# Kernel optimization log

Measured on AMD Instinct MI355X. Metric: run time of the kernel, lower is better.

The kernel has to match this reference:

```python
import jax, jax.numpy as jnp
import numpy as np

N_BOXES = 512
NUM_CLASSES = 151
IN_DIM = 4096
NMS_THRESH = 0.3


def setup_inputs() -> dict:
    key = jax.random.key(0)
    k1, k2, k3, k4 = jax.random.split(key, 4)
    obj_fmap = jax.random.normal(k1, (N_BOXES, IN_DIM), dtype=jnp.float32)
    W = jax.random.normal(k2, (IN_DIM, NUM_CLASSES), dtype=jnp.float32) * 0.02
    b = jnp.zeros((NUM_CLASSES,), dtype=jnp.float32)
    xy = jax.random.uniform(k3, (N_BOXES, NUM_CLASSES, 2), minval=0.0, maxval=800.0)
    wh = jax.random.uniform(k4, (N_BOXES, NUM_CLASSES, 2), minval=20.0, maxval=220.0)
    boxes_per_cls = jnp.concatenate([xy, xy + wh], axis=-1).astype(jnp.float32)
    return {"obj_fmap": obj_fmap, "boxes_per_cls": boxes_per_cls, "W": W, "b": b}


def nms_overlaps(boxes):
    # boxes: [N, C, 4] xyxy -> per-class pairwise IoU [N, N, C]
    x1, y1, x2, y2 = boxes[..., 0], boxes[..., 1], boxes[..., 2], boxes[..., 3]
    areas = (x2 - x1 + 1.0) * (y2 - y1 + 1.0)  # [N, C]
    ix1 = jnp.maximum(x1[:, None, :], x1[None, :, :])  # [N, N, C]
    iy1 = jnp.maximum(y1[:, None, :], y1[None, :, :])
    ix2 = jnp.minimum(x2[:, None, :], x2[None, :, :])
    iy2 = jnp.minimum(y2[:, None, :], y2[None, :, :])
    iw = jnp.clip(ix2 - ix1 + 1.0, 0.0)
    ih = jnp.clip(iy2 - iy1 + 1.0, 0.0)
    inter = iw * ih
    union = areas[:, None, :] + areas[None, :, :] - inter
    return inter / union


def greedy_nms_decode(obj_dists, boxes_per_cls, thresh):
    # Sequential greedy commitment: repeatedly take global argmax over the
    # [N, C] score matrix, commit that class to that box, zero out the same
    # class for overlapping boxes, and retire the committed box.
    N, C = obj_dists.shape
    is_overlap = nms_overlaps(boxes_per_cls) >= thresh  # [N, N, C] bool
    scores = jax.nn.softmax(obj_dists, axis=1)
    scores = scores.at[:, 0].set(0.0)  # never pick background

    def step(carry, _):
        scores, commits = carry
        flat = jnp.argmax(scores)
        box = flat // C
        cls = flat % C
        commits = commits.at[box].set(cls)
        col = jnp.where(is_overlap[box, :, cls], 0.0, scores[:, cls])
        scores = scores.at[:, cls].set(col)
        scores = scores.at[box].set(-1.0)
        return (scores, commits), None

    init = (scores, jnp.zeros((N,), dtype=jnp.int32))
    (_, commits), _ = jax.lax.scan(step, init, None, length=N)
    return commits


def reference(obj_fmap, boxes_per_cls, W, b):
    # out_obj linear head
    obj_dists = obj_fmap @ W + b  # [N, C]
    # sgdet eval path: greedy NMS-style class commitment
    obj_preds = greedy_nms_decode(obj_dists, boxes_per_cls, NMS_THRESH)
    return (obj_dists, obj_preds)
```

## Files before the change

### kernel.cpp

```cpp
#include <hip/hip_runtime.h>
#include <limits.h>

#pragma clang fp contract(off)

#define NB 512
#define NC 151
#define KDIM 4096
#define KS 8
#define KCH (KDIM/KS)
#define GRB 4
#define PST 152
#define NK 64
#define NL 16
#define CMX 16
#define RMX 64
#define NMS_TH 0.3f

typedef unsigned long long ull;

__device__ __forceinline__ bool overlap_ge(const float4& c, const float4& o) {
  float areaC = (c.z - c.x + 1.0f) * (c.w - c.y + 1.0f);
  float areaJ = (o.z - o.x + 1.0f) * (o.w - o.y + 1.0f);
  float iw = fminf(c.z, o.z) - fmaxf(c.x, o.x) + 1.0f;
  float ih = fminf(c.w, o.w) - fmaxf(c.y, o.y) + 1.0f;
  iw = fmaxf(iw, 0.0f); ih = fmaxf(ih, 0.0f);
  float inter = iw * ih;
  float uni = areaC + areaJ - inter;
  return inter / uni >= NMS_TH;
}

__device__ __forceinline__ bool mbit(const unsigned m[5], int c) {
  bool r = false;
#pragma unroll
  for (int k = 0; k < 5; ++k) r = (k == (c >> 5)) ? (((m[k] >> (c & 31)) & 1u) != 0) : r;
  return r;
}

__device__ __forceinline__ ull shflx_u64(ull v, int m) {
  int lo = (int)(unsigned)(v & 0xFFFFFFFFull);
  int hi = (int)(unsigned)(v >> 32);
  lo = __shfl_xor(lo, m, 64);
  hi = __shfl_xor(hi, m, 64);
  return ((ull)(unsigned)hi << 32) | (unsigned)lo;
}

__device__ __forceinline__ ull readlane_u64(ull v, int t) {
  int lo = __builtin_amdgcn_readlane((int)(unsigned)(v & 0xFFFFFFFFull), t);
  int hi = __builtin_amdgcn_readlane((int)(unsigned)(v >> 32), t);
  return ((ull)(unsigned)hi << 32) | (unsigned)lo;
}

#define TPB_GEMM ((NB / GRB) * KS)
#define NTR ((NB * NC + 191) / 192)
__global__ __launch_bounds__(192) void gemm_fused(
    const float* __restrict__ A, const float* __restrict__ W,
    const float* __restrict__ boxes, float* __restrict__ part, float* __restrict__ bt)
{
  if (blockIdx.x >= TPB_GEMM) {
    int i = (blockIdx.x - TPB_GEMM) * 192 + threadIdx.x;
    if (i < NB * NC) {
      int r = i / NC, c = i - r * NC;
      float4 v = *(const float4*)(boxes + (size_t)i * 4);
      *(float4*)(bt + ((size_t)c * NB + r) * 4) = v;
    }
    return;
  }
  __shared__ float sA[GRB * KCH];
  int rb = blockIdx.x >> 3, ks = blockIdx.x & 7;
  const float* Ab = A + (size_t)rb * GRB * KDIM + (size_t)ks * KCH;
  for (int i = threadIdx.x; i < GRB * (KCH / 4); i += 192) {
    int r = i >> 7;
    int k4 = i & 127;
    *(float4*)(sA + r * KCH + k4 * 4) = *(const float4*)(Ab + (size_t)r * KDIM + k4 * 4);
  }
  __syncthreads();
  int c = threadIdx.x;
  if (c < NC) {
    const float* wp = W + (size_t)ks * KCH * NC + c;
    float acc[GRB];
#pragma unroll
    for (int r = 0; r < GRB; ++r) acc[r] = 0.f;
    float w0 = wp[0], w1 = wp[NC], w2 = wp[2 * NC], w3 = wp[3 * NC];
    for (int k4 = 0; k4 < KCH / 4; ++k4) {
      int kn = (k4 + 1 < KCH / 4) ? (k4 + 1) : k4;
      const float* q = wp + (size_t)(4 * kn) * NC;
      float n0 = q[0], n1 = q[NC], n2 = q[2 * NC], n3 = q[3 * NC];
#pragma unroll
      for (int r = 0; r < GRB; ++r) {
        float4 a = *(const float4*)(sA + r * KCH + k4 * 4);
        acc[r] = fmaf(a.x, w0, acc[r]);
        acc[r] = fmaf(a.y, w1, acc[r]);
        acc[r] = fmaf(a.z, w2, acc[r]);
        acc[r] = fmaf(a.w, w3, acc[r]);
      }
      w0 = n0; w1 = n1; w2 = n2; w3 = n3;
    }
    float* o = part + ((size_t)ks * NB + (size_t)rb * GRB) * PST + c;
#pragma unroll
    for (int r = 0; r < GRB; ++r) o[(size_t)r * PST] = acc[r];
  }
}

__global__ __launch_bounds__(64) void prep_kernel(
    const float* __restrict__ part, const float* __restrict__ bias,
    float* __restrict__ out, float* __restrict__ lp, float* __restrict__ tl)
{
  const int j = blockIdx.x;
  const int l = threadIdx.x;
  const int c0 = l, c1 = l + 64, c2 = l + 128;
  const bool v2 = (c2 < NC);

  float x0 = 0.f, x1 = 0.f, x2 = 0.f;
#pragma unroll
  for (int ks = 0; ks < KS; ++ks) {
    const float* pb = part + ((size_t)ks * NB + j) * PST;
    x0 += pb[c0];
    x1 += pb[c1];
    if (v2) x2 += pb[c2];
  }
  x0 += bias[c0];
  x1 += bias[c1];
  if (v2) x2 += bias[c2]; else x2 = -3.4e38f;

  float* orow = out + (size_t)j * NC;
  orow[c0] = x0;
  orow[c1] = x1;
  if (v2) orow[c2] = x2;

  float m_ = fmaxf(x0, fmaxf(x1, x2));
#pragma unroll
  for (int d = 1; d < 64; d <<= 1) m_ = fmaxf(m_, __shfl_xor(m_, d, 64));

  float e0 = expf(x0 - m_), e1 = expf(x1 - m_), e2 = expf(x2 - m_);
  float s_ = e0 + e1 + e2;
#pragma unroll
  for (int d = 1; d < 64; d <<= 1) s_ += __shfl_xor(s_, d, 64);

  float p0 = (c0 == 0) ? 0.f : e0 / s_;
  float p1 = e1 / s_;
  float p2 = e2 / s_;

  float* pr = lp + (size_t)j * PST;
  pr[c0] = p0;
  pr[c1] = p1;
  if (c2 < PST) pr[c2] = v2 ? p2 : 0.f;

  auto mk = [&](float p, int c) -> ull {
    if (!(p > 0.f)) return 0ull;
    unsigned u = __float_as_uint(p) ^ 0x80000000u;
    return ((ull)u << 32) | (unsigned)(255 - c);
  };
  ull k0 = mk(p0, c0), k1 = mk(p1, c1), k2 = v2 ? mk(p2, c2) : 0ull;
  { ull a = k0 > k1 ? k0 : k1, b = k0 > k1 ? k1 : k0; k0 = a; k1 = b; }
  { ull a = k1 > k2 ? k1 : k2, b = k1 > k2 ? k2 : k1; k1 = a; k2 = b; }
  { ull a = k0 > k1 ? k0 : k1, b = k0 > k1 ? k1 : k0; k0 = a; k1 = b; }

  ull mykey = 0ull;
#pragma unroll
  for (int t = 0; t < NL; ++t) {
    ull g = k0;
#pragma unroll
    for (int d = 1; d < 64; d <<= 1) {
      ull o = shflx_u64(g, d);
      g = g > o ? g : o;
    }
    if (g != 0ull && k0 == g) { k0 = k1; k1 = k2; k2 = 0ull; }
    if (l == t) mykey = g;
  }

  if (l < NL) {
    float lv; int lc;
    if (mykey == 0ull) { lv = -3.4e38f; lc = 0; }
    else {
      lv = __uint_as_float((unsigned)(mykey >> 32) ^ 0x80000000u);
      lc = 255 - (int)(mykey & 0xFFu);
    }
    float* tr = tl + (size_t)j * (2 * NL);
    tr[l] = lv;
    tr[NL + l] = __int_as_float(lc);
  }
}

__global__ __launch_bounds__(192) void gemm_full(
    const float* __restrict__ A, const float* __restrict__ W,
    const float* __restrict__ bias, float* __restrict__ out)
{
  int c = threadIdx.x;
  int r0 = blockIdx.x * 4;
  if (c >= NC) return;
  const float* a = A + (size_t)r0 * KDIM;
  const float* wp = W + c;
  float a0 = 0.f, a1 = 0.f, a2 = 0.f, a3 = 0.f;
#pragma unroll 8
  for (int k = 0; k < KDIM; ++k) {
    float w = wp[(size_t)k * NC];
    a0 = fmaf(a[k],            w, a0);
    a1 = fmaf(a[k + KDIM],     w, a1);
    a2 = fmaf(a[k + 2 * KDIM], w, a2);
    a3 = fmaf(a[k + 3 * KDIM], w, a3);
  }
  float bb = bias[c];
  out[(size_t)(r0 + 0) * NC + c] = a0 + bb;
  out[(size_t)(r0 + 1) * NC + c] = a1 + bb;
  out[(size_t)(r0 + 2) * NC + c] = a2 + bb;
  out[(size_t)(r0 + 3) * NC + c] = a3 + bb;
}

template <bool FAST>
__global__ __launch_bounds__(512) void decode_kernel(
    const float* __restrict__ lp, const float* __restrict__ tl,
    const float* __restrict__ boxes ,
    float* __restrict__ commits)
{
  __shared__ __align__(16) ull bufA[NB];
  __shared__ __align__(16) ull bufB[NB];
  __shared__ __align__(16) int swin[NK];
  __shared__ ull smask[NK];
  __shared__ unsigned slog[NB];
  __shared__ int cls_cnt[NC];
  __shared__ unsigned short cls_ref[NC][CMX];
  __shared__ unsigned short P[NB];
  __shared__ ull nkk[RMX];
  __shared__ int nkr[RMX], nko[RMX], nkc[RMX];
  __shared__ int m_cnt;
  __shared__ ull sred[8];
  const int j = threadIdx.x;
  const int lane = j & 63;
  const int w = j >> 6;

  auto bload = [&](int cls, int row) -> float4 {
    return FAST ? *(const float4*)(boxes + ((size_t)cls * NB + row) * 4)
                : *(const float4*)(boxes + ((size_t)row * NC + cls) * 4);
  };
  auto enc = [&](float v, int cls) -> ull {
    unsigned u = __float_as_uint(v);
    u ^= (u & 0x80000000u) ? 0xFFFFFFFFu : 0x80000000u;
    return ((ull)u << 32) | (unsigned)(0xFFFFFFFFu - (unsigned)(j * NC + cls));
  };

  if (j < NC) cls_cnt[j] = 0;

  float lv[NL]; int lc[NL];
  float m_ = 0.f, s_ = 1.f;
  const float* xr = FAST ? (lp + (size_t)j * PST) : (lp + (size_t)j * NC);

  if (FAST) {
    const float4* tl4 = (const float4*)(tl + (size_t)j * (2 * NL));
#pragma unroll
    for (int q = 0; q < NL / 4; ++q) {
      float4 v = tl4[q];
      lv[4 * q] = v.x; lv[4 * q + 1] = v.y; lv[4 * q + 2] = v.z; lv[4 * q + 3] = v.w;
    }
#pragma unroll
    for (int q = 0; q < NL / 4; ++q) {
      float4 v = tl4[NL / 4 + q];
      lc[4 * q] = __float_as_int(v.x); lc[4 * q + 1] = __float_as_int(v.y);
      lc[4 * q + 2] = __float_as_int(v.z); lc[4 * q + 3] = __float_as_int(v.w);
    }
  } else {
#pragma unroll
    for (int t = 0; t < NL; ++t) { lv[t] = -3.4e38f; lc[t] = 0; }
    m_ = xr[0];
    for (int c = 1; c < NC; ++c) m_ = fmaxf(m_, xr[c]);
    s_ = 0.f;
    for (int c = 0; c < NC; ++c) s_ += expf(xr[c] - m_);
    for (int c = 1; c < NC; ++c) {
      float v = expf(xr[c] - m_) / s_;
      if (v > lv[NL - 1]) {
        lv[NL - 1] = v; lc[NL - 1] = c;
#pragma unroll
        for (int q = NL - 1; q > 0; --q) {
          if (lv[q] > lv[q - 1]) {
            float tv = lv[q]; lv[q] = lv[q - 1]; lv[q - 1] = tv;
            int tc = lc[q]; lc[q] = lc[q - 1]; lc[q - 1] = tc;
          }
        }
      }
    }
  }

  float rowmax; int argcls; bool zstuck = false;
  if (lv[0] > 0.f) { rowmax = lv[0]; argcls = lc[0]; }
  else { rowmax = 0.f; argcls = 0; zstuck = true; }

  bool retired = false;
  int commitcls = 0;
  int ncom = 0;
  int base = 0;
  int logcnt = 0;
  int flip = 0;
  bool eg = false;

  auto fullsort = [&](ull key) {
    __syncthreads();
    bufB[j] = key;
    __syncthreads();
    int rank = 0;
#pragma unroll 8
    for (int q = 0; q < NB; ++q) rank += (bufB[q] > key) ? 1 : 0;
    bufA[rank] = key;
    P[j] = (unsigned short)rank;
    __syncthreads();
  };

  fullsort(enc(rowmax, argcls));

  while (ncom < NB) {
    ull* Lc = flip ? bufB : bufA;
    ull* Ln = flip ? bufA : bufB;
    int bsz = NB - base; if (bsz > NK) bsz = NK;
    int myprev = (!retired && !zstuck) ? cls_cnt[argcls] : 0;

    if (j < bsz) {
      ull k = Lc[base + j];
      unsigned f = 0xFFFFFFFFu - (unsigned)k;
      int row = (int)(f / (unsigned)NC);
      swin[j] = (row << 8) | (int)(f - (unsigned)row * (unsigned)NC);
      smask[j] = 0ull;
    }
    if (j == 0) m_cnt = 0;
    if (w == 7) {
      volatile int* pb = (volatile int*)slog;
      int t0 = pb[(lane & 31) * 16];
      int t1 = pb[(lane & 31) * 16 + 1];
      asm volatile("" :: "v"(t0), "v"(t1));
    }
    __syncthreads();

    {
      int t = j >> 3, sb = (j & 7) * 8;
      if (t < bsz) {
        int pT = swin[t];
        int cT = pT & 255, rT = pT >> 8;
        int4 sA4 = *(const int4*)&swin[sb];
        int4 sB4 = *(const int4*)&swin[sb + 4];
        int ss[8] = {sA4.x, sA4.y, sA4.z, sA4.w, sB4.x, sB4.y, sB4.z, sB4.w};
        ull myc = 0ull;
#pragma unroll
        for (int u = 0; u < 8; ++u) {
          int s = sb + u;
          if (s < t && (ss[u] & 255) == cT) {
            float4 bs = bload(cT, ss[u] >> 8);
            float4 btx = bload(cT, rT);
            if (overlap_ge(bs, btx)) myc |= (1ull << s);
          }
        }
        if (myc) atomicOr(&smask[t], myc);
      }
    }
    __syncthreads();

    int p;
    {
      ull kv = (lane < bsz) ? Lc[base + lane] : 0ull;
      ull sm = (lane < bsz) ? smask[lane] : 0ull;
      ull okm = __ballot((lane < bsz) && ((unsigned)(kv >> 32) > 0x80000000u));
      ull anyc = __ballot(sm != 0ull);
      if (!(okm & 1ull)) {
        p = 0; eg = true;
      } else if (anyc == 0ull) {
        ull inv = ~okm;
        if (inv == 0ull) p = 64;
        else p = (int)__ffsll((long long)inv) - 1;
        eg = (p < bsz);
      } else {
        ull valid = 1ull; p = 1;
#pragma unroll
        for (int t = 1; t < NK; ++t) {
          ull cm = readlane_u64(sm, t);
          bool ok = (p == t) && ((okm >> t) & 1ull) && ((cm & valid) == 0ull);
          if (ok) { valid |= (1ull << t); p = t + 1; }
        }
        eg = (p < bsz) && !((okm >> p) & 1ull);
      }
    }

    if (j < p) {
      unsigned e = (unsigned)swin[j];
      slog[logcnt + j] = e;
      int c = (int)(e & 255u);
      int old = atomicAdd(&cls_cnt[c], 1);
      if (old < CMX) cls_ref[c][old] = (unsigned short)(logcnt + j);
    }
    __syncthreads();
    logcnt += p;

    bool chg = false; ull nkey = 0ull;
    if (!retired) {
      int mypos = (int)P[j];
      if (mypos >= base && mypos < base + p) {
        retired = true; commitcls = argcls;
      } else if (!zstuck) {
        bool supp = false;
        int nowc = cls_cnt[argcls];
        if (nowc > myprev) {
          float4 ob = bload(argcls, j);
          if (nowc <= CMX) {
#pragma unroll 1
            for (int q = myprev; q < nowc && !supp; ++q) {
              unsigned e = slog[cls_ref[argcls][q]];
              if (overlap_ge(bload(argcls, (int)(e >> 8)), ob)) supp = true;
            }
          } else {
#pragma unroll 1
            for (int q = logcnt - p; q < logcnt && !supp; ++q) {
              unsigned e = slog[q];
              if ((int)(e & 255u) == argcls &&
                  overlap_ge(bload(argcls, (int)(e >> 8)), ob)) supp = true;
            }
          }
        }
        if (supp) {
          bool found = false;
#pragma unroll 1
          for (int t = 0; t < NL && !found; ++t) {
            if (!(lv[t] > 0.f)) break;
            int c = lc[t];
            int cnt = cls_cnt[c];
            bool bad = false;
            if (cnt > 0) {
              float4 ob2 = bload(c, j);
              if (cnt <= CMX) {
                for (int q = 0; q < cnt && !bad; ++q) {
                  unsigned e = slog[cls_ref[c][q]];
                  if (overlap_ge(bload(c, (int)(e >> 8)), ob2)) bad = true;
                }
              } else {
                for (int q = 0; q < logcnt && !bad; ++q) {
                  unsigned e = slog[q];
                  if ((int)(e & 255u) == c &&
                      overlap_ge(bload(c, (int)(e >> 8)), ob2)) bad = true;
                }
              }
            }
            if (!bad) { rowmax = lv[t]; argcls = c; found = true; }
          }
          if (!found) {
            unsigned msk[5] = {0, 0, 0, 0, 0};
            for (int q = 0; q < logcnt; ++q) {
              unsigned e = slog[q];
              int c = (int)(e & 255u), r = (int)(e >> 8);
              if (r != j && !mbit(msk, c)) {
                if (overlap_ge(bload(c, r), bload(c, j))) {
#pragma unroll
                  for (int k5b = 0; k5b < 5; ++k5b)
                    if (k5b == (c >> 5)) msk[k5b] |= (1u << (c & 31));
                }
              }
            }
            float bm = -3.4e38f; int ba = 0;
            if (FAST) {
              for (int c4 = 0; c4 < PST / 4; ++c4) {
                float4 v4 = *(const float4*)(xr + c4 * 4);
                int c = c4 * 4;
                float vals[4] = {v4.x, v4.y, v4.z, v4.w};
#pragma unroll
                for (int u = 0; u < 4; ++u) {
                  int cc = c + u;
                  float v = mbit(msk, cc) ? 0.f : vals[u];
                  if (v > bm) { bm = v; ba = cc; }
                }
              }
            } else {
              for (int c = 0; c < NC; ++c) {
                float v;
                if (c == 0) v = 0.f;
                else v = mbit(msk, c) ? 0.f : (expf(xr[c] - m_) / s_);
                if (v > bm) { bm = v; ba = c; }
              }
            }
            rowmax = bm; argcls = ba;
            if (!(bm > 0.f)) zstuck = true;
          }
          chg = true; nkey = enc(rowmax, argcls);
        }
      }
    }
    if (chg) {
      int i = atomicAdd(&m_cnt, 1);
      if (i < RMX) { nkk[i] = nkey; nkr[i] = j; nko[i] = (int)P[j]; nkc[i] = 0; }
    }
    __syncthreads();

    int m = m_cnt;
    base += p; ncom += p;
    if (eg) break;
    if (m == 0) continue;

    if (m <= RMX) {
      bool haveslot = (j >= base);
      ull myk = 0ull; bool isrem = false; int rb_ = 0;
      if (haveslot) {
        myk = Lc[j];
#pragma unroll 1
        for (int i = 0; i < m; ++i) { int op = nko[i]; isrem |= (op == j); rb_ += (op < j) ? 1 : 0; }
      }
#pragma unroll 1
      for (int i = 0; i < m; ++i) {
        ull b = __ballot(haveslot && !isrem && (myk > nkk[i]));
        if (lane == 0 && b) atomicAdd(&nkc[i], (int)__popcll(b));
      }
      if (haveslot && !isrem) {
        int nb_ = 0;
#pragma unroll 1
        for (int i = 0; i < m; ++i) nb_ += (nkk[i] > myk) ? 1 : 0;
        int np = j - rb_ + nb_;
        Ln[np] = myk;
        if (myk != 0ull) {
          unsigned f = 0xFFFFFFFFu - (unsigned)myk;
          int rr = (int)(f / (unsigned)NC);
          P[rr] = (unsigned short)np;
        }
      }
      __syncthreads();
      if (j < m) {
        ull ki = nkk[j]; int gt = 0;
#pragma unroll 1
        for (int i = 0; i < m; ++i) gt += (nkk[i] > ki) ? 1 : 0;
        int np = base + nkc[j] + gt;
        Ln[np] = ki;
        P[nkr[j]] = (unsigned short)np;
      }
      __syncthreads();
      flip ^= 1;
    } else {
      fullsort(enc(rowmax, argcls));
      flip = 0;
      base = 0;
    }
  }

  if (ncom < NB) {
    unsigned msk[5] = {0, 0, 0, 0, 0};
    int post_min = INT_MAX;
    bool ret = false; int ccls = commitcls;
    for (int q = 0; q < logcnt; ++q) {
      unsigned e = slog[q];
      int r = (int)(e >> 8), c = (int)(e & 255u);
      if (j == r) { ret = true; ccls = c; post_min = INT_MAX; }
      else {
        if (overlap_ge(bload(c, r), bload(c, j))) {
          if (ret) post_min = (c < post_min) ? c : post_min;
          else {
#pragma unroll
            for (int k5b = 0; k5b < 5; ++k5b) if (k5b == (c >> 5)) msk[k5b] |= (1u << (c & 31));
          }
        }
      }
    }
    retired = ret; if (ret) commitcls = ccls;
    if (retired) {
      rowmax = (post_min != INT_MAX) ? 0.0f : -1.0f;
      argcls = (post_min != INT_MAX) ? post_min : 0;
    } else {
      float bm = -3.4e38f; int ba = 0;
      if (FAST) {
        for (int c4 = 0; c4 < PST / 4; ++c4) {
          float4 v4 = *(const float4*)(xr + c4 * 4);
          int c = c4 * 4;
          float vals[4] = {v4.x, v4.y, v4.z, v4.w};
#pragma unroll
          for (int u = 0; u < 4; ++u) {
            int cc = c + u;
            float v = mbit(msk, cc) ? 0.f : vals[u];
            if (v > bm) { bm = v; ba = cc; }
          }
        }
      } else {
        for (int c = 0; c < NC; ++c) {
          float v;
          if (c == 0) v = 0.f;
          else v = mbit(msk, c) ? 0.f : (expf(xr[c] - m_) / s_);
          if (v > bm) { bm = v; ba = c; }
        }
      }
      rowmax = bm; argcls = ba;
    }

    while (ncom < NB) {
      ull k = enc(rowmax, argcls);
#pragma unroll
      for (int dd = 32; dd >= 1; dd >>= 1) {
        ull o = shflx_u64(k, dd);
        k = k > o ? k : o;
      }
      __syncthreads();
      if (lane == 0) sred[w] = k;
      if (w == 7) {
        volatile int* pb = (volatile int*)slog;
        int t0 = pb[(lane & 31) * 16];
        asm volatile("" :: "v"(t0));
      }
      __syncthreads();
      ull g = sred[0];
#pragma unroll
      for (int q = 1; q < 8; ++q) { ull t = sred[q]; g = g > t ? g : t; }
      unsigned f = 0xFFFFFFFFu - (unsigned)g;
      int row = (int)(f / (unsigned)NC);
      int cls = (int)(f - (unsigned)row * (unsigned)NC);
      float4 cb = bload(cls, row);
      float4 ob = bload(cls, j);
      if (j == row) {
        retired = true; commitcls = cls;
        rowmax = -1.0f; argcls = 0;
        post_min = INT_MAX;
      } else if (overlap_ge(cb, ob)) {
        if (retired) {
          post_min = (cls < post_min) ? cls : post_min;
          rowmax = 0.0f; argcls = post_min;
        }
      }
      ++ncom;
    }
  }

  commits[j] = (float)commitcls;
}

extern "C" void kernel_launch(void* const* d_in, const int* in_sizes, int n_in,
                              void* d_out, int out_size, void* d_ws, size_t ws_size,
                              hipStream_t stream) {
  const float* A     = (const float*)d_in[0];
  const float* boxes = (const float*)d_in[1];
  const float* W     = (const float*)d_in[2];
  const float* bias  = (const float*)d_in[3];
  float* out = (float*)d_out;

  const size_t np = (size_t)KS * NB * PST;
  const size_t nl = (size_t)NB * PST;
  const size_t nt = (size_t)NB * (2 * NL);
  const size_t nb = (size_t)NC * NB * 4;
  const size_t need = (np + nl + nt + nb) * 4;

  if (ws_size >= need) {
    float* part = (float*)d_ws;
    float* lp   = part + np;
    float* tl   = lp + nl;
    float* bt   = tl + nt;
    gemm_fused<<<TPB_GEMM + NTR, 192, 0, stream>>>(A, W, boxes, part, bt);
    prep_kernel<<<NB, 64, 0, stream>>>(part, bias, out, lp, tl);
    decode_kernel<true><<<1, NB, 0, stream>>>(lp, tl, bt, out + NB * NC);
  } else {
    gemm_full<<<NB / 4, 192, 0, stream>>>(A, W, bias, out);
    decode_kernel<false><<<1, NB, 0, stream>>>(out, nullptr, boxes, out + NB * NC);
  }
}
```

Before: 139.7 us.

## Fuse GEMM, softmax prep and greedy decode into one cooperative kernel

Replaces the three-kernel sequence (split-K GEMM plus box transpose, prep/softmax/top-16, single-block decode) with one cooperative launch of 512 blocks of 512 threads. Grid-wide syncs separate the phases. The GEMM phase is retiled to 8 rows per block with register prefetch of W. This removes two kernel-launch gaps, but it adds grid-sync cost and leaves 511 blocks idle during the serial decode. If the cooperative launch fails, the old three-kernel path runs instead.

```diff
diff --git a/kernel.cpp b/kernel.cpp
--- a/kernel.cpp
+++ b/kernel.cpp
@@ -1,7 +1,10 @@
 #include <hip/hip_runtime.h>
+#include <hip/hip_cooperative_groups.h>
 #include <limits.h>
 
 #pragma clang fp contract(off)
+
+namespace cg = cooperative_groups;
 
 #define NB 512
 #define NC 151
@@ -48,6 +51,509 @@
   int lo = __builtin_amdgcn_readlane((int)(unsigned)(v & 0xFFFFFFFFull), t);
   int hi = __builtin_amdgcn_readlane((int)(unsigned)(v >> 32), t);
   return ((ull)(unsigned)hi << 32) | (unsigned)lo;
+}
+
+__global__ __launch_bounds__(512) void fused_kernel(
+    const float* __restrict__ A, const float* __restrict__ W,
+    const float* __restrict__ boxes, const float* __restrict__ bias,
+    float* __restrict__ part, float* __restrict__ lp, float* __restrict__ tl,
+    float* __restrict__ bt, float* __restrict__ out)
+{
+  __shared__ float sA[8 * KCH];
+  __shared__ __align__(16) ull bufA[NB];
+  __shared__ __align__(16) ull bufB[NB];
+  __shared__ __align__(16) int swin[NK];
+  __shared__ ull smask[NK];
+  __shared__ unsigned slog[NB];
+  __shared__ int cls_cnt[NC];
+  __shared__ unsigned short cls_ref[NC][CMX];
+  __shared__ unsigned short P[NB];
+  __shared__ ull nkk[RMX];
+  __shared__ int nkr[RMX], nko[RMX], nkc[RMX];
+  __shared__ int m_cnt;
+  __shared__ ull sred[8];
+
+  const int bid = blockIdx.x;
+  const int t = threadIdx.x;
+
+  {
+    int rb = bid >> 3, ks = bid & 7;
+    const float* Ab = A + (size_t)rb * 8 * KDIM + (size_t)ks * KCH;
+    for (int i = t; i < 8 * (KCH / 4); i += 512) {
+      int r = i >> 7, k4 = i & 127;
+      *(float4*)(sA + r * KCH + k4 * 4) = *(const float4*)(Ab + (size_t)r * KDIM + k4 * 4);
+    }
+    int ti = bid * 512 + t;
+    if (ti < NB * NC) {
+      int r = ti / NC, c = ti - r * NC;
+      float4 v = *(const float4*)(boxes + (size_t)ti * 4);
+      *(float4*)(bt + ((size_t)c * NB + r) * 4) = v;
+    }
+    __syncthreads();
+    int c = t & 255, h = t >> 8;
+    if (c < NC) {
+      const float* wp = W + (size_t)ks * KCH * NC + c;
+      float acc[4];
+#pragma unroll
+      for (int r = 0; r < 4; ++r) acc[r] = 0.f;
+      const float* sb = sA + (size_t)(h * 4) * KCH;
+      float w0 = wp[0], w1 = wp[NC], w2 = wp[2 * NC], w3 = wp[3 * NC];
+      for (int k4 = 0; k4 < KCH / 4; ++k4) {
+        int kn = (k4 + 1 < KCH / 4) ? (k4 + 1) : k4;
+        const float* q = wp + (size_t)(4 * kn) * NC;
+        float n0 = q[0], n1 = q[NC], n2 = q[2 * NC], n3 = q[3 * NC];
+#pragma unroll
+        for (int r = 0; r < 4; ++r) {
+          float4 a = *(const float4*)(sb + r * KCH + k4 * 4);
+          acc[r] = fmaf(a.x, w0, acc[r]);
+          acc[r] = fmaf(a.y, w1, acc[r]);
+          acc[r] = fmaf(a.z, w2, acc[r]);
+          acc[r] = fmaf(a.w, w3, acc[r]);
+        }
+        w0 = n0; w1 = n1; w2 = n2; w3 = n3;
+      }
+      float* o = part + ((size_t)ks * NB + (size_t)rb * 8 + h * 4) * PST + c;
+#pragma unroll
+      for (int r = 0; r < 4; ++r) o[(size_t)r * PST] = acc[r];
+    }
+  }
+
+  cg::this_grid().sync();
+
+  if (bid < 64) {
+    const int wv = t >> 6, l = t & 63;
+    const int j = bid * 8 + wv;
+    const int c0 = l, c1 = l + 64, c2 = l + 128;
+    const bool v2 = (c2 < NC);
+
+    float x0 = 0.f, x1 = 0.f, x2 = 0.f;
+#pragma unroll
+    for (int ks = 0; ks < KS; ++ks) {
+      const float* pb = part + ((size_t)ks * NB + j) * PST;
+      x0 += pb[c0];
+      x1 += pb[c1];
+      if (v2) x2 += pb[c2];
+    }
+    x0 += bias[c0];
+    x1 += bias[c1];
+    if (v2) x2 += bias[c2]; else x2 = -3.4e38f;
+
+    float* orow = out + (size_t)j * NC;
+    orow[c0] = x0;
+    orow[c1] = x1;
+    if (v2) orow[c2] = x2;
+
+    float m_ = fmaxf(x0, fmaxf(x1, x2));
+#pragma unroll
+    for (int d = 1; d < 64; d <<= 1) m_ = fmaxf(m_, __shfl_xor(m_, d, 64));
+
+    float e0 = expf(x0 - m_), e1 = expf(x1 - m_), e2 = expf(x2 - m_);
+    float s_ = e0 + e1 + e2;
+#pragma unroll
+    for (int d = 1; d < 64; d <<= 1) s_ += __shfl_xor(s_, d, 64);
+
+    float p0 = (c0 == 0) ? 0.f : e0 / s_;
+    float p1 = e1 / s_;
+    float p2 = e2 / s_;
+
+    float* pr = lp + (size_t)j * PST;
+    pr[c0] = p0;
+    pr[c1] = p1;
+    if (c2 < PST) pr[c2] = v2 ? p2 : 0.f;
+
+    auto mk = [&](float p, int c) -> ull {
+      if (!(p > 0.f)) return 0ull;
+      unsigned u = __float_as_uint(p) ^ 0x80000000u;
+      return ((ull)u << 32) | (unsigned)(255 - c);
+    };
+    ull k0 = mk(p0, c0), k1 = mk(p1, c1), k2 = v2 ? mk(p2, c2) : 0ull;
+    { ull a = k0 > k1 ? k0 : k1, b = k0 > k1 ? k1 : k0; k0 = a; k1 = b; }
+    { ull a = k1 > k2 ? k1 : k2, b = k1 > k2 ? k2 : k1; k1 = a; k2 = b; }
+    { ull a = k0 > k1 ? k0 : k1, b = k0 > k1 ? k1 : k0; k0 = a; k1 = b; }
+
+    ull mykey = 0ull;
+#pragma unroll
+    for (int tt = 0; tt < NL; ++tt) {
+      ull g = k0;
+#pragma unroll
+      for (int d = 1; d < 64; d <<= 1) {
+        ull o = shflx_u64(g, d);
+        g = g > o ? g : o;
+      }
+      if (g != 0ull && k0 == g) { k0 = k1; k1 = k2; k2 = 0ull; }
+      if (l == tt) mykey = g;
+    }
+
+    if (l < NL) {
+      float lvv; int lcc;
+      if (mykey == 0ull) { lvv = -3.4e38f; lcc = 0; }
+      else {
+        lvv = __uint_as_float((unsigned)(mykey >> 32) ^ 0x80000000u);
+        lcc = 255 - (int)(mykey & 0xFFu);
+      }
+      float* tr = tl + (size_t)j * (2 * NL);
+      tr[l] = lvv;
+      tr[NL + l] = __int_as_float(lcc);
+    }
+  }
+
+  cg::this_grid().sync();
+
+  if (bid != 0) return;
+  {
+    const int j = t;
+    const int lane = j & 63;
+    const int w = j >> 6;
+    float* commits = out + NB * NC;
+
+    auto bload = [&](int cls, int row) -> float4 {
+      return *(const float4*)(bt + ((size_t)cls * NB + row) * 4);
+    };
+    auto enc = [&](float v, int cls) -> ull {
+      unsigned u = __float_as_uint(v);
+      u ^= (u & 0x80000000u) ? 0xFFFFFFFFu : 0x80000000u;
+      return ((ull)u << 32) | (unsigned)(0xFFFFFFFFu - (unsigned)(j * NC + cls));
+    };
+
+    if (j < NC) cls_cnt[j] = 0;
+
+    float lv[NL]; int lc[NL];
+    const float* xr = lp + (size_t)j * PST;
+
+    {
+      const float4* tl4 = (const float4*)(tl + (size_t)j * (2 * NL));
+#pragma unroll
+      for (int q = 0; q < NL / 4; ++q) {
+        float4 v = tl4[q];
+        lv[4 * q] = v.x; lv[4 * q + 1] = v.y; lv[4 * q + 2] = v.z; lv[4 * q + 3] = v.w;
+      }
+#pragma unroll
+      for (int q = 0; q < NL / 4; ++q) {
+        float4 v = tl4[NL / 4 + q];
+        lc[4 * q] = __float_as_int(v.x); lc[4 * q + 1] = __float_as_int(v.y);
+        lc[4 * q + 2] = __float_as_int(v.z); lc[4 * q + 3] = __float_as_int(v.w);
+      }
+    }
+
+    float rowmax; int argcls; bool zstuck = false;
+    if (lv[0] > 0.f) { rowmax = lv[0]; argcls = lc[0]; }
+    else { rowmax = 0.f; argcls = 0; zstuck = true; }
+
+    bool retired = false;
+    int commitcls = 0;
+    int ncom = 0;
+    int base = 0;
+    int logcnt = 0;
+    int flip = 0;
+    bool eg = false;
+
+    auto fullsort = [&](ull key) {
+      __syncthreads();
+      bufB[j] = key;
+      __syncthreads();
+      int rank = 0;
+#pragma unroll 8
+      for (int q = 0; q < NB; ++q) rank += (bufB[q] > key) ? 1 : 0;
+      bufA[rank] = key;
+      P[j] = (unsigned short)rank;
+      __syncthreads();
+    };
+
+    fullsort(enc(rowmax, argcls));
+
+    while (ncom < NB) {
+      ull* Lc = flip ? bufB : bufA;
+      ull* Ln = flip ? bufA : bufB;
+      int bsz = NB - base; if (bsz > NK) bsz = NK;
+      int myprev = (!retired && !zstuck) ? cls_cnt[argcls] : 0;
+
+      if (j < bsz) {
+        ull k = Lc[base + j];
+        unsigned f = 0xFFFFFFFFu - (unsigned)k;
+        int row = (int)(f / (unsigned)NC);
+        swin[j] = (row << 8) | (int)(f - (unsigned)row * (unsigned)NC);
+        smask[j] = 0ull;
+      }
+      if (j == 0) m_cnt = 0;
+      if (w == 7) {
+        volatile int* pb = (volatile int*)slog;
+        int t0 = pb[(lane & 31) * 16];
+        int t1 = pb[(lane & 31) * 16 + 1];
+        asm volatile("" :: "v"(t0), "v"(t1));
+      }
+      __syncthreads();
+
+      {
+        int tt = j >> 3, sb = (j & 7) * 8;
+        if (tt < bsz) {
+          int pT = swin[tt];
+          int cT = pT & 255, rT = pT >> 8;
+          int4 sA4 = *(const int4*)&swin[sb];
+          int4 sB4 = *(const int4*)&swin[sb + 4];
+          int ss[8] = {sA4.x, sA4.y, sA4.z, sA4.w, sB4.x, sB4.y, sB4.z, sB4.w};
+          ull myc = 0ull;
+#pragma unroll
+          for (int u = 0; u < 8; ++u) {
+            int s = sb + u;
+            if (s < tt && (ss[u] & 255) == cT) {
+              float4 bs = bload(cT, ss[u] >> 8);
+              float4 btx = bload(cT, rT);
+              if (overlap_ge(bs, btx)) myc |= (1ull << s);
+            }
+          }
+          if (myc) atomicOr(&smask[tt], myc);
+        }
+      }
+      __syncthreads();
+
+      int p;
+      {
+        ull kv = (lane < bsz) ? Lc[base + lane] : 0ull;
+        ull sm = (lane < bsz) ? smask[lane] : 0ull;
+        ull okm = __ballot((lane < bsz) && ((unsigned)(kv >> 32) > 0x80000000u));
+        ull anyc = __ballot(sm != 0ull);
+        if (!(okm & 1ull)) {
+          p = 0; eg = true;
+        } else if (anyc == 0ull) {
+          ull inv = ~okm;
+          if (inv == 0ull) p = 64;
+          else p = (int)__ffsll((long long)inv) - 1;
+          eg = (p < bsz);
+        } else {
+          ull valid = 1ull; p = 1;
+#pragma unroll
+          for (int tt = 1; tt < NK; ++tt) {
+            ull cm = readlane_u64(sm, tt);
+            bool ok = (p == tt) && ((okm >> tt) & 1ull) && ((cm & valid) == 0ull);
+            if (ok) { valid |= (1ull << tt); p = tt + 1; }
+          }
+          eg = (p < bsz) && !((okm >> p) & 1ull);
+        }
+      }
+
+      if (j < p) {
+        unsigned e = (unsigned)swin[j];
+        slog[logcnt + j] = e;
+        int c = (int)(e & 255u);
+        int old = atomicAdd(&cls_cnt[c], 1);
+        if (old < CMX) cls_ref[c][old] = (unsigned short)(logcnt + j);
+      }
+      __syncthreads();
+      logcnt += p;
+
+      bool chg = false; ull nkey = 0ull;
+      if (!retired) {
+        int mypos = (int)P[j];
+        if (mypos >= base && mypos < base + p) {
+          retired = true; commitcls = argcls;
+        } else if (!zstuck) {
+          bool supp = false;
+          int nowc = cls_cnt[argcls];
+          if (nowc > myprev) {
+            float4 ob = bload(argcls, j);
+            if (nowc <= CMX) {
+#pragma unroll 1
+              for (int q = myprev; q < nowc && !supp; ++q) {
+                unsigned e = slog[cls_ref[argcls][q]];
+                if (overlap_ge(bload(argcls, (int)(e >> 8)), ob)) supp = true;
+              }
+            } else {
+#pragma unroll 1
+              for (int q = logcnt - p; q < logcnt && !supp; ++q) {
+                unsigned e = slog[q];
+                if ((int)(e & 255u) == argcls &&
+                    overlap_ge(bload(argcls, (int)(e >> 8)), ob)) supp = true;
+              }
+            }
+          }
+          if (supp) {
+            bool found = false;
+#pragma unroll 1
+            for (int tt = 0; tt < NL && !found; ++tt) {
+              if (!(lv[tt] > 0.f)) break;
+              int c = lc[tt];
+              int cnt = cls_cnt[c];
+              bool bad = false;
+              if (cnt > 0) {
+                float4 ob2 = bload(c, j);
+                if (cnt <= CMX) {
+                  for (int q = 0; q < cnt && !bad; ++q) {
+                    unsigned e = slog[cls_ref[c][q]];
+                    if (overlap_ge(bload(c, (int)(e >> 8)), ob2)) bad = true;
+                  }
+                } else {
+                  for (int q = 0; q < logcnt && !bad; ++q) {
+                    unsigned e = slog[q];
+                    if ((int)(e & 255u) == c &&
+                        overlap_ge(bload(c, (int)(e >> 8)), ob2)) bad = true;
+                  }
+                }
+              }
+              if (!bad) { rowmax = lv[tt]; argcls = c; found = true; }
+            }
+            if (!found) {
+              unsigned msk[5] = {0, 0, 0, 0, 0};
+              for (int q = 0; q < logcnt; ++q) {
+                unsigned e = slog[q];
+                int c = (int)(e & 255u), r = (int)(e >> 8);
+                if (r != j && !mbit(msk, c)) {
+                  if (overlap_ge(bload(c, r), bload(c, j))) {
+#pragma unroll
+                    for (int k5b = 0; k5b < 5; ++k5b)
+                      if (k5b == (c >> 5)) msk[k5b] |= (1u << (c & 31));
+                  }
+                }
+              }
+              float bm = -3.4e38f; int ba = 0;
+              for (int c4 = 0; c4 < PST / 4; ++c4) {
+                float4 v4 = *(const float4*)(xr + c4 * 4);
+                int c = c4 * 4;
+                float vals[4] = {v4.x, v4.y, v4.z, v4.w};
+#pragma unroll
+                for (int u = 0; u < 4; ++u) {
+                  int cc = c + u;
+                  float v = mbit(msk, cc) ? 0.f : vals[u];
+                  if (v > bm) { bm = v; ba = cc; }
+                }
+              }
+              rowmax = bm; argcls = ba;
+              if (!(bm > 0.f)) zstuck = true;
+            }
+            chg = true; nkey = enc(rowmax, argcls);
+          }
+        }
+      }
+      if (chg) {
+        int i = atomicAdd(&m_cnt, 1);
+        if (i < RMX) { nkk[i] = nkey; nkr[i] = j; nko[i] = (int)P[j]; nkc[i] = 0; }
+      }
+      __syncthreads();
+
+      int m = m_cnt;
+      base += p; ncom += p;
+      if (eg) break;
+      if (m == 0) continue;
+
+      if (m <= RMX) {
+        bool haveslot = (j >= base);
+        ull myk = 0ull; bool isrem = false; int rb_ = 0;
+        if (haveslot) {
+          myk = Lc[j];
+#pragma unroll 1
+          for (int i = 0; i < m; ++i) { int op = nko[i]; isrem |= (op == j); rb_ += (op < j) ? 1 : 0; }
+        }
+#pragma unroll 1
+        for (int i = 0; i < m; ++i) {
+          ull b = __ballot(haveslot && !isrem && (myk > nkk[i]));
+          if (lane == 0 && b) atomicAdd(&nkc[i], (int)__popcll(b));
+        }
+        if (haveslot && !isrem) {
+          int nb_ = 0;
+#pragma unroll 1
+          for (int i = 0; i < m; ++i) nb_ += (nkk[i] > myk) ? 1 : 0;
+          int np = j - rb_ + nb_;
+          Ln[np] = myk;
+          if (myk != 0ull) {
+            unsigned f = 0xFFFFFFFFu - (unsigned)myk;
+            int rr = (int)(f / (unsigned)NC);
+            P[rr] = (unsigned short)np;
+          }
+        }
+        __syncthreads();
+        if (j < m) {
+          ull ki = nkk[j]; int gt = 0;
+#pragma unroll 1
+          for (int i = 0; i < m; ++i) gt += (nkk[i] > ki) ? 1 : 0;
+          int np = base + nkc[j] + gt;
+          Ln[np] = ki;
+          P[nkr[j]] = (unsigned short)np;
+        }
+        __syncthreads();
+        flip ^= 1;
+      } else {
+        fullsort(enc(rowmax, argcls));
+        flip = 0;
+        base = 0;
+      }
+    }
+
+    if (ncom < NB) {
+      unsigned msk[5] = {0, 0, 0, 0, 0};
+      int post_min = INT_MAX;
+      bool ret = false; int ccls = commitcls;
+      for (int q = 0; q < logcnt; ++q) {
+        unsigned e = slog[q];
+        int r = (int)(e >> 8), c = (int)(e & 255u);
+        if (j == r) { ret = true; ccls = c; post_min = INT_MAX; }
+        else {
+          if (overlap_ge(bload(c, r), bload(c, j))) {
+            if (ret) post_min = (c < post_min) ? c : post_min;
+            else {
+#pragma unroll
+              for (int k5b = 0; k5b < 5; ++k5b) if (k5b == (c >> 5)) msk[k5b] |= (1u << (c & 31));
+            }
+          }
+        }
+      }
+      retired = ret; if (ret) commitcls = ccls;
+      if (retired) {
+        rowmax = (post_min != INT_MAX) ? 0.0f : -1.0f;
+        argcls = (post_min != INT_MAX) ? post_min : 0;
+      } else {
+        float bm = -3.4e38f; int ba = 0;
+        for (int c4 = 0; c4 < PST / 4; ++c4) {
+          float4 v4 = *(const float4*)(xr + c4 * 4);
+          int c = c4 * 4;
+          float vals[4] = {v4.x, v4.y, v4.z, v4.w};
+#pragma unroll
+          for (int u = 0; u < 4; ++u) {
+            int cc = c + u;
+            float v = mbit(msk, cc) ? 0.f : vals[u];
+            if (v > bm) { bm = v; ba = cc; }
+          }
+        }
+        rowmax = bm; argcls = ba;
+      }
+
+      while (ncom < NB) {
+        ull k = enc(rowmax, argcls);
+#pragma unroll
+        for (int dd = 32; dd >= 1; dd >>= 1) {
+          ull o = shflx_u64(k, dd);
+          k = k > o ? k : o;
+        }
+        __syncthreads();
+        if (lane == 0) sred[w] = k;
+        if (w == 7) {
+          volatile int* pb = (volatile int*)slog;
+          int t0 = pb[(lane & 31) * 16];
+          asm volatile("" :: "v"(t0));
+        }
+        __syncthreads();
+        ull g = sred[0];
+#pragma unroll
+        for (int q = 1; q < 8; ++q) { ull tt = sred[q]; g = g > tt ? g : tt; }
+        unsigned f = 0xFFFFFFFFu - (unsigned)g;
+        int row = (int)(f / (unsigned)NC);
+        int cls = (int)(f - (unsigned)row * (unsigned)NC);
+        float4 cb = bload(cls, row);
+        float4 ob = bload(cls, j);
+        if (j == row) {
+          retired = true; commitcls = cls;
+          rowmax = -1.0f; argcls = 0;
+          post_min = INT_MAX;
+        } else if (overlap_ge(cb, ob)) {
+          if (retired) {
+            post_min = (cls < post_min) ? cls : post_min;
+            rowmax = 0.0f; argcls = post_min;
+          }
+        }
+        ++ncom;
+      }
+    }
+
+    commits[j] = (float)commitcls;
+  }
 }
 
 #define TPB_GEMM ((NB / GRB) * KS)
@@ -209,8 +715,7 @@
 template <bool FAST>
 __global__ __launch_bounds__(512) void decode_kernel(
     const float* __restrict__ lp, const float* __restrict__ tl,
-    const float* __restrict__ boxes ,
-    float* __restrict__ commits)
+    const float* __restrict__ boxes, float* __restrict__ commits)
 {
   __shared__ __align__(16) ull bufA[NB];
   __shared__ __align__(16) ull bufB[NB];
@@ -637,9 +1142,15 @@
     float* lp   = part + np;
     float* tl   = lp + nl;
     float* bt   = tl + nt;
-    gemm_fused<<<TPB_GEMM + NTR, 192, 0, stream>>>(A, W, boxes, part, bt);
-    prep_kernel<<<NB, 64, 0, stream>>>(part, bias, out, lp, tl);
-    decode_kernel<true><<<1, NB, 0, stream>>>(lp, tl, bt, out + NB * NC);
+    void* args[] = { (void*)&A, (void*)&W, (void*)&boxes, (void*)&bias,
+                     (void*)&part, (void*)&lp, (void*)&tl, (void*)&bt, (void*)&out };
+    hipError_t e = hipLaunchCooperativeKernel((const void*)fused_kernel,
+                                              dim3(512), dim3(512), args, 0, stream);
+    if (e != hipSuccess) {
+      gemm_fused<<<TPB_GEMM + NTR, 192, 0, stream>>>(A, W, boxes, part, bt);
+      prep_kernel<<<NB, 64, 0, stream>>>(part, bias, out, lp, tl);
+      decode_kernel<true><<<1, NB, 0, stream>>>(lp, tl, bt, out + NB * NC);
+    }
   } else {
     gemm_full<<<NB / 4, 192, 0, stream>>>(A, W, bias, out);
     decode_kernel<false><<<1, NB, 0, stream>>>(out, nullptr, boxes, out + NB * NC);
```

Result: slower. 260.0 us (+86.2%).

## Widen greedy decode window and resolve the accepted prefix via first-conflict atomics

Applied to the files above, without the earlier changes.

Raises the per-round candidate window of the greedy decode from 64 to 256 entries. The per-pair conflict bitmask and the serial readlane chain walk are replaced by two shared atomicMin values: the first non-positive score and the first candidate that overlaps any earlier same-class candidate. The accepted prefix is the minimum of the two. This cuts the number of sequential rounds and the serial resolution step. In exchange, each thread-pair scans up to 128 earlier candidates per round, with global box loads inside the loop.

```diff
diff --git a/kernel.cpp b/kernel.cpp
--- a/kernel.cpp
+++ b/kernel.cpp
@@ -10,7 +10,7 @@
 #define KCH (KDIM/KS)
 #define GRB 4
 #define PST 152
-#define NK 64
+#define NK 256
 #define NL 16
 #define CMX 16
 #define RMX 64
@@ -41,12 +41,6 @@
   int hi = (int)(unsigned)(v >> 32);
   lo = __shfl_xor(lo, m, 64);
   hi = __shfl_xor(hi, m, 64);
-  return ((ull)(unsigned)hi << 32) | (unsigned)lo;
-}
-
-__device__ __forceinline__ ull readlane_u64(ull v, int t) {
-  int lo = __builtin_amdgcn_readlane((int)(unsigned)(v & 0xFFFFFFFFull), t);
-  int hi = __builtin_amdgcn_readlane((int)(unsigned)(v >> 32), t);
   return ((ull)(unsigned)hi << 32) | (unsigned)lo;
 }
 
@@ -214,8 +208,7 @@
 {
   __shared__ __align__(16) ull bufA[NB];
   __shared__ __align__(16) ull bufB[NB];
-  __shared__ __align__(16) int swin[NK];
-  __shared__ ull smask[NK];
+  __shared__ int swin[NK];
   __shared__ unsigned slog[NB];
   __shared__ int cls_cnt[NC];
   __shared__ unsigned short cls_ref[NC][CMX];
@@ -223,6 +216,7 @@
   __shared__ ull nkk[RMX];
   __shared__ int nkr[RMX], nko[RMX], nkc[RMX];
   __shared__ int m_cnt;
+  __shared__ int s_fb, s_fc;
   __shared__ ull sred[8];
   const int j = threadIdx.x;
   const int lane = j & 63;
@@ -311,14 +305,14 @@
     int bsz = NB - base; if (bsz > NK) bsz = NK;
     int myprev = (!retired && !zstuck) ? cls_cnt[argcls] : 0;
 
+    ull mykb = 0ull;
     if (j < bsz) {
-      ull k = Lc[base + j];
-      unsigned f = 0xFFFFFFFFu - (unsigned)k;
+      mykb = Lc[base + j];
+      unsigned f = 0xFFFFFFFFu - (unsigned)mykb;
       int row = (int)(f / (unsigned)NC);
       swin[j] = (row << 8) | (int)(f - (unsigned)row * (unsigned)NC);
-      smask[j] = 0ull;
-    }
-    if (j == 0) m_cnt = 0;
+    }
+    if (j == 0) { m_cnt = 0; s_fb = NK; s_fc = NK; }
     if (w == 7) {
       volatile int* pb = (volatile int*)slog;
       int t0 = pb[(lane & 31) * 16];
@@ -327,53 +321,30 @@
     }
     __syncthreads();
 
+    if (j < bsz && !((unsigned)(mykb >> 32) > 0x80000000u))
+      atomicMin(&s_fb, j);
     {
-      int t = j >> 3, sb = (j & 7) * 8;
-      if (t < bsz) {
+      int t = j >> 1, hf = (j & 1) * 128;
+      if (t > 0 && t < bsz) {
         int pT = swin[t];
         int cT = pT & 255, rT = pT >> 8;
-        int4 sA4 = *(const int4*)&swin[sb];
-        int4 sB4 = *(const int4*)&swin[sb + 4];
-        int ss[8] = {sA4.x, sA4.y, sA4.z, sA4.w, sB4.x, sB4.y, sB4.z, sB4.w};
-        ull myc = 0ull;
-#pragma unroll
-        for (int u = 0; u < 8; ++u) {
-          int s = sb + u;
-          if (s < t && (ss[u] & 255) == cT) {
-            float4 bs = bload(cT, ss[u] >> 8);
+        int smax = (t < hf + 128) ? t : (hf + 128);
+        bool hit = false;
+        for (int s = hf; s < smax && !hit; ++s) {
+          if ((swin[s] & 255) == cT) {
+            float4 bs = bload(cT, swin[s] >> 8);
             float4 btx = bload(cT, rT);
-            if (overlap_ge(bs, btx)) myc |= (1ull << s);
+            if (overlap_ge(bs, btx)) hit = true;
           }
         }
-        if (myc) atomicOr(&smask[t], myc);
+        if (hit) atomicMin(&s_fc, t);
       }
     }
     __syncthreads();
 
-    int p;
-    {
-      ull kv = (lane < bsz) ? Lc[base + lane] : 0ull;
-      ull sm = (lane < bsz) ? smask[lane] : 0ull;
-      ull okm = __ballot((lane < bsz) && ((unsigned)(kv >> 32) > 0x80000000u));
-      ull anyc = __ballot(sm != 0ull);
-      if (!(okm & 1ull)) {
-        p = 0; eg = true;
-      } else if (anyc == 0ull) {
-        ull inv = ~okm;
-        if (inv == 0ull) p = 64;
-        else p = (int)__ffsll((long long)inv) - 1;
-        eg = (p < bsz);
-      } else {
-        ull valid = 1ull; p = 1;
-#pragma unroll
-        for (int t = 1; t < NK; ++t) {
-          ull cm = readlane_u64(sm, t);
-          bool ok = (p == t) && ((okm >> t) & 1ull) && ((cm & valid) == 0ull);
-          if (ok) { valid |= (1ull << t); p = t + 1; }
-        }
-        eg = (p < bsz) && !((okm >> p) & 1ull);
-      }
-    }
+    int fb = s_fb, fc = s_fc;
+    int p = fb < fc ? fb : fc; if (p > bsz) p = bsz;
+    eg = (p < bsz) && (fb <= fc);
 
     if (j < p) {
       unsigned e = (unsigned)swin[j];
```

After: 188.3 us. 34.8% more time.
